# Kernel optimization log

Measured on AMD Instinct MI355X. Metric: run time of the kernel, lower is better.

## Reference

```python
import jax, jax.numpy as jnp
import numpy as np

B, TQ, TK, D, H = 4, 2048, 2048, 512, 8  # hidden=512, num_heads=8, head_dim=64


def setup_inputs() -> dict:
    key = jax.random.key(0)
    ks = jax.random.split(key, 7)
    s = 0.03  # small init scale for linear weights
    return {
        "q": jax.random.normal(ks[0], (B, TQ, D), jnp.float32),
        "k": jax.random.normal(ks[1], (B, TK, D), jnp.float32),
        "v": jax.random.normal(ks[2], (B, TK, D), jnp.float32),
        "Wq": jax.random.normal(ks[3], (D, D), jnp.float32) * s,
        "bq": jnp.zeros((D,), jnp.float32),
        "Wk": jax.random.normal(ks[4], (D, D), jnp.float32) * s,
        "bk": jnp.zeros((D,), jnp.float32),
        "Wv": jax.random.normal(ks[5], (D, D), jnp.float32) * s,
        "bv": jnp.zeros((D,), jnp.float32),
        "Wo": jax.random.normal(ks[6], (D, D), jnp.float32) * s,
        "bo": jnp.zeros((D,), jnp.float32),
    }


def reference(q, k, v, Wq, bq, Wk, bk, Wv, bv, Wo, bo):
    Bq, Tq, _ = q.shape
    Tk = k.shape[1]
    Dh = D // H  # head dim = 64
    # torch Linear: x @ W.T + b; split heads -> [B, H, T, Dh]
    qh = (q @ Wq.T + bq).reshape(Bq, Tq, H, Dh).transpose(0, 2, 1, 3)
    kh = (k @ Wk.T + bk).reshape(Bq, Tk, H, Dh).transpose(0, 2, 1, 3)
    vh = (v @ Wv.T + bv).reshape(Bq, Tk, H, Dh).transpose(0, 2, 1, 3)
    scale = 1.0 / float(np.sqrt(Dh))
    scores = jnp.einsum("bhqd,bhkd->bhqk", qh, kh) * scale  # [B,H,Tq,Tk]
    # causal mask: tril(ones, diagonal=Tk-Tq); log-additive masking == -inf off-band
    causal = jnp.tril(jnp.ones((Tq, Tk), bool), k=Tk - Tq)
    scores = jnp.where(causal, scores, -jnp.inf)
    w = jax.nn.softmax(scores, axis=-1)  # attention weights
    x = jnp.einsum("bhqk,bhkd->bhqd", w, vh)
    x = x.transpose(0, 2, 1, 3).reshape(Bq, Tq, D)
    return x @ Wo.T + bo, w
```

## Files before the change

### kernel.cpp

```cpp
#include <hip/hip_runtime.h>


typedef __attribute__((ext_vector_type(4))) float f32x4;
typedef __attribute__((ext_vector_type(8))) short short8;
typedef __attribute__((ext_vector_type(8))) __bf16 bf16x8;
typedef __attribute__((ext_vector_type(2))) unsigned int uintx2;
typedef __attribute__((ext_vector_type(4))) unsigned int uintx4;

static __device__ __forceinline__ unsigned short bfc(float f) {
  return __builtin_bit_cast(unsigned short, (__bf16)f);
}
static __device__ __forceinline__ unsigned pkbf(float a, float b) {
  return (unsigned)bfc(a) | ((unsigned)bfc(b) << 16);
}
static __device__ __forceinline__ short8 cvt_bf8(f32x4 f0, f32x4 f1) {
  uintx4 u;
  u[0] = pkbf(f0[0], f0[1]);
  u[1] = pkbf(f0[2], f0[3]);
  u[2] = pkbf(f1[0], f1[1]);
  u[3] = pkbf(f1[2], f1[3]);
  return __builtin_bit_cast(short8, u);
}

static __device__ __forceinline__ f32x4 mfma16(short8 a, short8 b, f32x4 c) {
  return __builtin_amdgcn_mfma_f32_16x16x32_bf16(
      __builtin_bit_cast(bf16x8, a), __builtin_bit_cast(bf16x8, b), c, 0, 0, 0);
}

#define GLD16(gsrc, ldst)                                                     \
  __builtin_amdgcn_global_load_lds(                                           \
      (const __attribute__((address_space(1))) void*)(gsrc),                  \
      (__attribute__((address_space(3))) void*)(ldst), 16, 0, 0)

template <int IN_BF16>
__device__ __forceinline__ void gemm_core(const void* __restrict__ Xv,
                                          const float* __restrict__ W,
                                          short (*As)[72], short (*Bs)[72],
                                          int row0, int col0, f32x4 (&acc)[4][4]) {
  const int tid = threadIdx.x;
  const int lane = tid & 63;
  const int wv = tid >> 6, wm = wv >> 1, wn = wv & 1;
  const int g = lane >> 4, c = lane & 15;

  for (int k0 = 0; k0 < 512; k0 += 64) {
    for (int ch = tid; ch < 1024; ch += 256) {
      const int r = ch >> 3, kc = (ch & 7) * 8;
      if (IN_BF16) {
        *(short8*)&As[r][kc] =
            *(const short8*)((const short*)Xv + (size_t)(row0 + r) * 512 + k0 + kc);
      } else {
        const float* src = (const float*)Xv + (size_t)(row0 + r) * 512 + k0 + kc;
        *(short8*)&As[r][kc] = cvt_bf8(*(const f32x4*)src, *(const f32x4*)(src + 4));
      }
      {
        const float* src = W + (size_t)(col0 + r) * 512 + k0 + kc;
        *(short8*)&Bs[r][kc] = cvt_bf8(*(const f32x4*)src, *(const f32x4*)(src + 4));
      }
    }
    __syncthreads();
#pragma unroll
    for (int kk = 0; kk < 2; ++kk) {
      short8 a[4], b[4];
#pragma unroll
      for (int i = 0; i < 4; ++i) a[i] = *(const short8*)&As[wm * 64 + i * 16 + c][kk * 32 + g * 8];
#pragma unroll
      for (int i = 0; i < 4; ++i) b[i] = *(const short8*)&Bs[wn * 64 + i * 16 + c][kk * 32 + g * 8];
#pragma unroll
      for (int mi = 0; mi < 4; ++mi)
#pragma unroll
        for (int ni = 0; ni < 4; ++ni) acc[mi][ni] = mfma16(a[mi], b[ni], acc[mi][ni]);
    }
    __syncthreads();
  }
}

__global__ __launch_bounds__(256) void qkv_gemm(
    const float* __restrict__ q, const float* __restrict__ k, const float* __restrict__ v,
    const float* __restrict__ Wq, const float* __restrict__ bq,
    const float* __restrict__ Wk, const float* __restrict__ bk,
    const float* __restrict__ Wv, const float* __restrict__ bv,
    unsigned short* __restrict__ Qbf, unsigned short* __restrict__ Kbf,
    unsigned short* __restrict__ Vbf) {
  __shared__ short As[128][72];
  __shared__ short Bs[128][72];
  const int z = blockIdx.z;
  const float* X = z == 0 ? q : (z == 1 ? k : v);
  const float* W = z == 0 ? Wq : (z == 1 ? Wk : Wv);
  const float* bias = z == 0 ? bq : (z == 1 ? bk : bv);
  const int row0 = blockIdx.x * 128, col0 = blockIdx.y * 128;

  f32x4 acc[4][4] = {};
  gemm_core<0>(X, W, As, Bs, row0, col0, acc);

  const int lane = threadIdx.x & 63;
  const int wv = threadIdx.x >> 6, wm = wv >> 1, wn = wv & 1;
  const int g = lane >> 4, c = lane & 15;

  if (z < 2) {
    unsigned short* Y = z == 0 ? Qbf : Kbf;
    const float scl = z == 0 ? 0.18033688f : 1.0f;
#pragma unroll
    for (int mi = 0; mi < 4; ++mi)
#pragma unroll
      for (int ni = 0; ni < 4; ++ni) {
        const int col = col0 + wn * 64 + ni * 16 + c;
        const float bvl = bias[col];
        const int rowb = row0 + wm * 64 + mi * 16 + g * 4;
#pragma unroll
        for (int r = 0; r < 4; ++r) {
          const int row = rowb + r;
          const int bb = row >> 11, t = row & 2047;
          const int h = col >> 6, dh = col & 63;
          Y[((size_t)((bb * 8 + h) * 2048 + t) << 6) + dh] = bfc((acc[mi][ni][r] + bvl) * scl);
        }
      }
  } else {
#pragma unroll
    for (int mi = 0; mi < 4; ++mi)
#pragma unroll
      for (int ni = 0; ni < 4; ++ni) {
        const int col = col0 + wn * 64 + ni * 16 + c;
        const float bvl = bias[col];
        const int rowb = row0 + wm * 64 + mi * 16 + g * 4;
        const int bb = rowb >> 11, t = rowb & 2047;
        const int h = col >> 6, dh = col & 63;
        uintx2 pk;
        pk[0] = pkbf(acc[mi][ni][0] + bvl, acc[mi][ni][1] + bvl);
        pk[1] = pkbf(acc[mi][ni][2] + bvl, acc[mi][ni][3] + bvl);
        *(uintx2*)(Vbf + ((size_t)((bb * 8 + h) * 64 + dh) * 2048 + t)) = pk;
      }
  }
}

__global__ __launch_bounds__(256) void out_gemm(const unsigned short* __restrict__ ctx,
                                                const float* __restrict__ Wo,
                                                const float* __restrict__ bo,
                                                float* __restrict__ out) {
  __shared__ short As[128][72];
  __shared__ short Bs[128][72];
  const int row0 = blockIdx.x * 128, col0 = blockIdx.y * 128;
  f32x4 acc[4][4] = {};
  gemm_core<1>(ctx, Wo, As, Bs, row0, col0, acc);

  const int lane = threadIdx.x & 63;
  const int wv = threadIdx.x >> 6, wm = wv >> 1, wn = wv & 1;
  const int g = lane >> 4, c = lane & 15;
#pragma unroll
  for (int mi = 0; mi < 4; ++mi)
#pragma unroll
    for (int ni = 0; ni < 4; ++ni) {
      const int col = col0 + wn * 64 + ni * 16 + c;
      const float bvl = bo[col];
      const int rowb = row0 + wm * 64 + mi * 16 + g * 4;
#pragma unroll
      for (int r = 0; r < 4; ++r) out[(size_t)(rowb + r) * 512 + col] = acc[mi][ni][r] + bvl;
    }
}

__global__ __launch_bounds__(256) void attn_kernel(
    const unsigned short* __restrict__ Qb, const unsigned short* __restrict__ Kb,
    const unsigned short* __restrict__ Vtg, unsigned short* __restrict__ ctx,
    float* __restrict__ wout) {
  __shared__ short Kd[2][8192];
  __shared__ short Vd[2][8192];
  __shared__ short Ps[4][16][128];

  const int tid = threadIdx.x, lane = tid & 63, wv = tid >> 6;
  const int g = lane >> 4, c = lane & 15;
  const int sw = (c & 7) << 3;
  const int p = blockIdx.x, bh = blockIdx.y;
  const unsigned short* Qp = Qb + (size_t)bh * (2048 * 64);
  const unsigned short* Kp = Kb + (size_t)bh * (2048 * 64);
  const unsigned short* Vp = Vtg + (size_t)bh * (64 * 2048);
  const int b_ = bh >> 3, h_ = bh & 7;

  for (int half = 0; half < 2; ++half) {
    const int t = half ? (31 - p) : p;
    const int q0 = t * 64;
    const int jmax = t >> 1;
    const int qr = q0 + wv * 16 + c;

    __syncthreads();
#pragma unroll
    for (int i = 0; i < 4; ++i) {
      const int gr = (wv * 4 + i) * 64 + lane;
      const int row = gr >> 3, slot = gr & 7;
      GLD16(Kp + ((size_t)row * 64) + ((slot ^ (row & 7)) << 3),
            (char*)Kd[0] + ((wv * 4 + i) << 10));
    }
#pragma unroll
    for (int i = 0; i < 4; ++i) {
      const int gr = (wv * 4 + i) * 64 + lane;
      const int row = gr >> 4, slot = gr & 15;
      GLD16(Vp + ((size_t)row * 2048) + ((slot ^ (row & 7)) << 3),
            (char*)Vd[0] + ((wv * 4 + i) << 10));
    }

    short8 qf[2];
    qf[0] = *(const short8*)(Qp + (size_t)qr * 64 + g * 8);
    qf[1] = *(const short8*)(Qp + (size_t)qr * 64 + 32 + g * 8);

    f32x4 O[4] = {};
    float l_r = 0.0f;

    for (int j = 0; j <= jmax; ++j) {
      __syncthreads();
      if (j < jmax) {
        const int nb = (j + 1) & 1;
#pragma unroll
        for (int i = 0; i < 4; ++i) {
          const int gr = (wv * 4 + i) * 64 + lane;
          const int row = gr >> 3, slot = gr & 7;
          GLD16(Kp + ((size_t)((j + 1) * 128 + row) * 64) + ((slot ^ (row & 7)) << 3),
                (char*)Kd[nb] + ((wv * 4 + i) << 10));
        }
#pragma unroll
        for (int i = 0; i < 4; ++i) {
          const int gr = (wv * 4 + i) * 64 + lane;
          const int row = gr >> 4, slot = gr & 15;
          GLD16(Vp + ((size_t)row * 2048) + (j + 1) * 128 + ((slot ^ (row & 7)) << 3),
                (char*)Vd[nb] + ((wv * 4 + i) << 10));
        }
      }
      const short* Ksb = Kd[j & 1];
      const short* Vsb = Vd[j & 1];

      f32x4 S[8];
#pragma unroll
      for (int nc = 0; nc < 8; ++nc) S[nc] = (f32x4){0.f, 0.f, 0.f, 0.f};
#pragma unroll
      for (int kk = 0; kk < 2; ++kk)
#pragma unroll
        for (int nc = 0; nc < 8; ++nc) {
          const int row = nc * 16 + c;
          const short8 kf = *(const short8*)&Ksb[row * 64 + (((kk * 4 + g) ^ (c & 7)) << 3)];
          S[nc] = mfma16(kf, qf[kk], S[nc]);
        }

      f32x4 ssum = {0.f, 0.f, 0.f, 0.f};
      if (j == jmax) {
        const int kvb = j * 128 + g * 4;
#pragma unroll
        for (int nc = 0; nc < 8; ++nc) {
#pragma unroll
          for (int r = 0; r < 4; ++r) {
            float val = __builtin_amdgcn_exp2f(S[nc][r]);
            if (kvb + nc * 16 + r > qr) val = 0.f;
            S[nc][r] = val;
          }
          ssum += S[nc];
        }
      } else {
#pragma unroll
        for (int nc = 0; nc < 8; ++nc) {
#pragma unroll
          for (int r = 0; r < 4; ++r) S[nc][r] = __builtin_amdgcn_exp2f(S[nc][r]);
          ssum += S[nc];
        }
      }
      l_r += ssum[0] + ssum[1] + ssum[2] + ssum[3];

#pragma unroll
      for (int nc = 0; nc < 8; ++nc) {
        uintx2 pk;
        pk[0] = pkbf(S[nc][0], S[nc][1]);
        pk[1] = pkbf(S[nc][2], S[nc][3]);
        *(uintx2*)&Ps[wv][c][(nc * 16 + g * 4) ^ sw] = pk;
      }

#pragma unroll
      for (int kk2 = 0; kk2 < 4; ++kk2) {
        const short8 pa = *(const short8*)&Ps[wv][c][(kk2 * 32 + g * 8) ^ sw];
#pragma unroll
        for (int nd = 0; nd < 4; ++nd) {
          const int row = nd * 16 + c;
          const short8 vb = *(const short8*)&Vsb[row * 128 + (((kk2 * 4 + g) ^ (c & 7)) << 3)];
          O[nd] = mfma16(pa, vb, O[nd]);
        }
      }
    }

    l_r += __shfl_xor(l_r, 16);
    l_r += __shfl_xor(l_r, 32);

    {
      float lv[4];
#pragma unroll
      for (int r = 0; r < 4; ++r) lv[r] = __shfl(l_r, g * 4 + r);
#pragma unroll
      for (int r = 0; r < 4; ++r) {
        const float inv = 1.0f / lv[r];
        const int trow = q0 + wv * 16 + g * 4 + r;
        unsigned short* cp = ctx + ((size_t)(b_ * 2048 + trow) * 512) + h_ * 64;
#pragma unroll
        for (int nd = 0; nd < 4; ++nd) cp[nd * 16 + c] = bfc(O[nd][r] * inv);
      }
    }

    const float inv_l = 1.0f / l_r;
    float* wbase = wout + ((size_t)bh * 2048 + q0) * 2048;
    for (int j = jmax; j >= 0; --j) {
      __syncthreads();
      if (j > 0) {
#pragma unroll
        for (int i = 0; i < 4; ++i) {
          const int gr = (wv * 4 + i) * 64 + lane;
          const int row = gr >> 3, slot = gr & 7;
          GLD16(Kp + ((size_t)((j - 1) * 128 + row) * 64) + ((slot ^ (row & 7)) << 3),
                (char*)Kd[(j - 1) & 1] + ((wv * 4 + i) << 10));
        }
      }
      const short* Ksb = Kd[j & 1];

      f32x4 S[8];
#pragma unroll
      for (int nc = 0; nc < 8; ++nc) S[nc] = (f32x4){0.f, 0.f, 0.f, 0.f};
#pragma unroll
      for (int kk = 0; kk < 2; ++kk)
#pragma unroll
        for (int nc = 0; nc < 8; ++nc) {
          const int row = nc * 16 + c;
          const short8 kf = *(const short8*)&Ksb[row * 64 + (((kk * 4 + g) ^ (c & 7)) << 3)];
          S[nc] = mfma16(kf, qf[kk], S[nc]);
        }

      const bool lastj = (j == jmax);
      float* wr = wbase + (size_t)(wv * 16 + c) * 2048 + j * 128;
#pragma unroll
      for (int nc = 0; nc < 8; ++nc) {
        f32x4 w4;
#pragma unroll
        for (int r = 0; r < 4; ++r) {
          float val = __builtin_amdgcn_exp2f(S[nc][r]) * inv_l;
          if (lastj && (j * 128 + nc * 16 + g * 4 + r > qr)) val = 0.f;
          w4[r] = val;
        }
        *(f32x4*)(wr + nc * 16 + g * 4) = w4;
      }
    }

    {
      const int c0 = (jmax + 1) * 128;
      const f32x4 z = {0.f, 0.f, 0.f, 0.f};
      for (int rr = wv; rr < 64; rr += 4) {
        float* rp = wbase + (size_t)rr * 2048;
        for (int x = c0 + lane * 4; x < 2048; x += 256) *(f32x4*)(rp + x) = z;
      }
    }
  }
}

extern "C" void kernel_launch(void* const* d_in, const int* in_sizes, int n_in,
                              void* d_out, int out_size, void* d_ws, size_t ws_size,
                              hipStream_t stream) {
  const float* q  = (const float*)d_in[0];
  const float* k  = (const float*)d_in[1];
  const float* v  = (const float*)d_in[2];
  const float* Wq = (const float*)d_in[3];
  const float* bq = (const float*)d_in[4];
  const float* Wk = (const float*)d_in[5];
  const float* bk = (const float*)d_in[6];
  const float* Wv = (const float*)d_in[7];
  const float* bv = (const float*)d_in[8];
  const float* Wo = (const float*)d_in[9];
  const float* bo = (const float*)d_in[10];

  unsigned short* Qbf = (unsigned short*)d_ws;
  unsigned short* Kbf = Qbf + (size_t)4194304;
  unsigned short* Vbf = Kbf + (size_t)4194304;
  unsigned short* ctx = Vbf + (size_t)4194304;

  float* out  = (float*)d_out;
  float* wout = out + (size_t)4 * 2048 * 512;

  qkv_gemm<<<dim3(64, 4, 3), 256, 0, stream>>>(q, k, v, Wq, bq, Wk, bk, Wv, bv, Qbf, Kbf, Vbf);
  attn_kernel<<<dim3(16, 32), 256, 0, stream>>>(Qbf, Kbf, Vbf, ctx, wout);
  out_gemm<<<dim3(64, 4), 256, 0, stream>>>(ctx, Wo, bo, out);
}
```

Before: 240.1 us.

## Pre-convert inputs to bf16, use async LDS loads in GEMMs, restructure attention grid

A separate conversion kernel turns the q/k/v activations and the projection weights into bf16, staging them in the attention-weights output buffer before it is overwritten. The QKV and output GEMMs then load their bf16 tiles straight into swizzled LDS with global_load_lds. The attention kernel drops the paired-tile scheme for one query tile per block on a larger grid with launch_bounds occupancy 3. It also reads V and the second-pass K directly from global memory instead of through LDS. The aim is less conversion work inside the GEMMs and higher attention occupancy, at the cost of an extra pass over the inputs and uncached global V/K loads.

```diff
diff --git a/kernel.cpp b/kernel.cpp
--- a/kernel.cpp
+++ b/kernel.cpp
@@ -32,39 +32,50 @@
       (const __attribute__((address_space(1))) void*)(gsrc),                  \
       (__attribute__((address_space(3))) void*)(ldst), 16, 0, 0)
 
-template <int IN_BF16>
-__device__ __forceinline__ void gemm_core(const void* __restrict__ Xv,
-                                          const float* __restrict__ W,
-                                          short (*As)[72], short (*Bs)[72],
-                                          int row0, int col0, f32x4 (&acc)[4][4]) {
-  const int tid = threadIdx.x;
-  const int lane = tid & 63;
+__global__ __launch_bounds__(256) void cvt_kernel(
+    const float* __restrict__ q, const float* __restrict__ k, const float* __restrict__ v,
+    const float* __restrict__ Wq, const float* __restrict__ Wk, const float* __restrict__ Wv,
+    unsigned short* __restrict__ dst) {
+  const int seg = blockIdx.y;
+  const float* src = seg == 0 ? q : seg == 1 ? k : seg == 2 ? v
+                     : seg == 3 ? Wq : seg == 4 ? Wk : Wv;
+  const size_t base = seg < 3 ? (size_t)seg * 4194304
+                              : 12582912ull + (size_t)(seg - 3) * 262144;
+  const size_t n = seg < 3 ? 4194304 : 262144;
+  const size_t i = ((size_t)blockIdx.x * 256 + threadIdx.x) * 8;
+  if (i < n) {
+    const f32x4 f0 = *(const f32x4*)(src + i), f1 = *(const f32x4*)(src + i + 4);
+    *(short8*)(dst + base + i) = cvt_bf8(f0, f1);
+  }
+}
+
+__device__ __forceinline__ void gemm_bf(const unsigned short* __restrict__ Xb,
+                                        const unsigned short* __restrict__ Wb,
+                                        short* As, short* Bs,
+                                        int row0, int col0, f32x4 (&acc)[4][4]) {
+  const int tid = threadIdx.x, lane = tid & 63;
   const int wv = tid >> 6, wm = wv >> 1, wn = wv & 1;
-  const int g = lane >> 4, c = lane & 15;
+  const int g = lane >> 4, c = lane & 15, sw = c & 7;
 
   for (int k0 = 0; k0 < 512; k0 += 64) {
-    for (int ch = tid; ch < 1024; ch += 256) {
-      const int r = ch >> 3, kc = (ch & 7) * 8;
-      if (IN_BF16) {
-        *(short8*)&As[r][kc] =
-            *(const short8*)((const short*)Xv + (size_t)(row0 + r) * 512 + k0 + kc);
-      } else {
-        const float* src = (const float*)Xv + (size_t)(row0 + r) * 512 + k0 + kc;
-        *(short8*)&As[r][kc] = cvt_bf8(*(const f32x4*)src, *(const f32x4*)(src + 4));
-      }
-      {
-        const float* src = W + (size_t)(col0 + r) * 512 + k0 + kc;
-        *(short8*)&Bs[r][kc] = cvt_bf8(*(const f32x4*)src, *(const f32x4*)(src + 4));
-      }
+#pragma unroll
+    for (int i = 0; i < 4; ++i) {
+      const int gr = (wv * 4 + i) * 64 + lane;
+      const int r = gr >> 3, s = gr & 7;
+      GLD16(Xb + (size_t)(row0 + r) * 512 + k0 + ((s ^ (r & 7)) << 3),
+            (char*)As + ((wv * 4 + i) << 10));
+      GLD16(Wb + (size_t)(col0 + r) * 512 + k0 + ((s ^ (r & 7)) << 3),
+            (char*)Bs + ((wv * 4 + i) << 10));
     }
     __syncthreads();
 #pragma unroll
     for (int kk = 0; kk < 2; ++kk) {
       short8 a[4], b[4];
 #pragma unroll
-      for (int i = 0; i < 4; ++i) a[i] = *(const short8*)&As[wm * 64 + i * 16 + c][kk * 32 + g * 8];
-#pragma unroll
-      for (int i = 0; i < 4; ++i) b[i] = *(const short8*)&Bs[wn * 64 + i * 16 + c][kk * 32 + g * 8];
+      for (int i = 0; i < 4; ++i) {
+        a[i] = *(const short8*)&As[((wm * 64 + i * 16 + c) << 6) + (((kk * 4 + g) ^ sw) << 3)];
+        b[i] = *(const short8*)&Bs[((wn * 64 + i * 16 + c) << 6) + (((kk * 4 + g) ^ sw) << 3)];
+      }
 #pragma unroll
       for (int mi = 0; mi < 4; ++mi)
 #pragma unroll
@@ -75,22 +86,20 @@
 }
 
 __global__ __launch_bounds__(256) void qkv_gemm(
-    const float* __restrict__ q, const float* __restrict__ k, const float* __restrict__ v,
-    const float* __restrict__ Wq, const float* __restrict__ bq,
-    const float* __restrict__ Wk, const float* __restrict__ bk,
-    const float* __restrict__ Wv, const float* __restrict__ bv,
+    const unsigned short* __restrict__ stash,
+    const float* __restrict__ bq, const float* __restrict__ bk, const float* __restrict__ bv,
     unsigned short* __restrict__ Qbf, unsigned short* __restrict__ Kbf,
     unsigned short* __restrict__ Vbf) {
-  __shared__ short As[128][72];
-  __shared__ short Bs[128][72];
+  __shared__ short As[128 * 64];
+  __shared__ short Bs[128 * 64];
   const int z = blockIdx.z;
-  const float* X = z == 0 ? q : (z == 1 ? k : v);
-  const float* W = z == 0 ? Wq : (z == 1 ? Wk : Wv);
+  const unsigned short* Xb = stash + (size_t)z * 4194304;
+  const unsigned short* Wb = stash + 12582912ull + (size_t)z * 262144;
   const float* bias = z == 0 ? bq : (z == 1 ? bk : bv);
   const int row0 = blockIdx.x * 128, col0 = blockIdx.y * 128;
 
   f32x4 acc[4][4] = {};
-  gemm_core<0>(X, W, As, Bs, row0, col0, acc);
+  gemm_bf(Xb, Wb, As, Bs, row0, col0, acc);
 
   const int lane = threadIdx.x & 63;
   const int wv = threadIdx.x >> 6, wm = wv >> 1, wn = wv & 1;
@@ -136,15 +145,44 @@
                                                 const float* __restrict__ Wo,
                                                 const float* __restrict__ bo,
                                                 float* __restrict__ out) {
-  __shared__ short As[128][72];
+  __shared__ short As[128 * 64];
   __shared__ short Bs[128][72];
+  const int tid = threadIdx.x, lane = tid & 63;
+  const int wv = tid >> 6, wm = wv >> 1, wn = wv & 1;
+  const int g = lane >> 4, c = lane & 15, sw = c & 7;
   const int row0 = blockIdx.x * 128, col0 = blockIdx.y * 128;
+
   f32x4 acc[4][4] = {};
-  gemm_core<1>(ctx, Wo, As, Bs, row0, col0, acc);
-
-  const int lane = threadIdx.x & 63;
-  const int wv = threadIdx.x >> 6, wm = wv >> 1, wn = wv & 1;
-  const int g = lane >> 4, c = lane & 15;
+  for (int k0 = 0; k0 < 512; k0 += 64) {
+#pragma unroll
+    for (int i = 0; i < 4; ++i) {
+      const int gr = (wv * 4 + i) * 64 + lane;
+      const int r = gr >> 3, s = gr & 7;
+      GLD16(ctx + (size_t)(row0 + r) * 512 + k0 + ((s ^ (r & 7)) << 3),
+            (char*)As + ((wv * 4 + i) << 10));
+    }
+    for (int ch = tid; ch < 1024; ch += 256) {
+      const int r = ch >> 3, kc = (ch & 7) * 8;
+      const float* src = Wo + (size_t)(col0 + r) * 512 + k0 + kc;
+      *(short8*)&Bs[r][kc] = cvt_bf8(*(const f32x4*)src, *(const f32x4*)(src + 4));
+    }
+    __syncthreads();
+#pragma unroll
+    for (int kk = 0; kk < 2; ++kk) {
+      short8 a[4], b[4];
+#pragma unroll
+      for (int i = 0; i < 4; ++i) {
+        a[i] = *(const short8*)&As[((wm * 64 + i * 16 + c) << 6) + (((kk * 4 + g) ^ sw) << 3)];
+        b[i] = *(const short8*)&Bs[wn * 64 + i * 16 + c][kk * 32 + g * 8];
+      }
+#pragma unroll
+      for (int mi = 0; mi < 4; ++mi)
+#pragma unroll
+        for (int ni = 0; ni < 4; ++ni) acc[mi][ni] = mfma16(a[mi], b[ni], acc[mi][ni]);
+    }
+    __syncthreads();
+  }
+
 #pragma unroll
   for (int mi = 0; mi < 4; ++mi)
 #pragma unroll
@@ -157,195 +195,163 @@
     }
 }
 
-__global__ __launch_bounds__(256) void attn_kernel(
+__global__ __launch_bounds__(256, 3) void attn_kernel(
     const unsigned short* __restrict__ Qb, const unsigned short* __restrict__ Kb,
     const unsigned short* __restrict__ Vtg, unsigned short* __restrict__ ctx,
     float* __restrict__ wout) {
   __shared__ short Kd[2][8192];
-  __shared__ short Vd[2][8192];
   __shared__ short Ps[4][16][128];
 
   const int tid = threadIdx.x, lane = tid & 63, wv = tid >> 6;
   const int g = lane >> 4, c = lane & 15;
   const int sw = (c & 7) << 3;
-  const int p = blockIdx.x, bh = blockIdx.y;
+  const int t = 31 - blockIdx.x, bh = blockIdx.y;
   const unsigned short* Qp = Qb + (size_t)bh * (2048 * 64);
   const unsigned short* Kp = Kb + (size_t)bh * (2048 * 64);
   const unsigned short* Vp = Vtg + (size_t)bh * (64 * 2048);
   const int b_ = bh >> 3, h_ = bh & 7;
 
-  for (int half = 0; half < 2; ++half) {
-    const int t = half ? (31 - p) : p;
-    const int q0 = t * 64;
-    const int jmax = t >> 1;
-    const int qr = q0 + wv * 16 + c;
-
-    __syncthreads();
-#pragma unroll
-    for (int i = 0; i < 4; ++i) {
-      const int gr = (wv * 4 + i) * 64 + lane;
-      const int row = gr >> 3, slot = gr & 7;
-      GLD16(Kp + ((size_t)row * 64) + ((slot ^ (row & 7)) << 3),
-            (char*)Kd[0] + ((wv * 4 + i) << 10));
-    }
-#pragma unroll
-    for (int i = 0; i < 4; ++i) {
-      const int gr = (wv * 4 + i) * 64 + lane;
-      const int row = gr >> 4, slot = gr & 15;
-      GLD16(Vp + ((size_t)row * 2048) + ((slot ^ (row & 7)) << 3),
-            (char*)Vd[0] + ((wv * 4 + i) << 10));
-    }
-
-    short8 qf[2];
-    qf[0] = *(const short8*)(Qp + (size_t)qr * 64 + g * 8);
-    qf[1] = *(const short8*)(Qp + (size_t)qr * 64 + 32 + g * 8);
-
-    f32x4 O[4] = {};
-    float l_r = 0.0f;
-
-    for (int j = 0; j <= jmax; ++j) {
-      __syncthreads();
-      if (j < jmax) {
-        const int nb = (j + 1) & 1;
-#pragma unroll
-        for (int i = 0; i < 4; ++i) {
-          const int gr = (wv * 4 + i) * 64 + lane;
-          const int row = gr >> 3, slot = gr & 7;
-          GLD16(Kp + ((size_t)((j + 1) * 128 + row) * 64) + ((slot ^ (row & 7)) << 3),
-                (char*)Kd[nb] + ((wv * 4 + i) << 10));
+  const int q0 = t * 64;
+  const int jmax = t >> 1;
+  const int qr = q0 + wv * 16 + c;
+
+#pragma unroll
+  for (int i = 0; i < 4; ++i) {
+    const int gr = (wv * 4 + i) * 64 + lane;
+    const int row = gr >> 3, slot = gr & 7;
+    GLD16(Kp + ((size_t)row * 64) + ((slot ^ (row & 7)) << 3),
+          (char*)Kd[0] + ((wv * 4 + i) << 10));
+  }
+
+  short8 qf[2];
+  qf[0] = *(const short8*)(Qp + (size_t)qr * 64 + g * 8);
+  qf[1] = *(const short8*)(Qp + (size_t)qr * 64 + 32 + g * 8);
+
+  f32x4 O[4] = {};
+  float l_r = 0.0f;
+
+  for (int j = 0; j <= jmax; ++j) {
+    __syncthreads();
+    if (j < jmax) {
+      const int nb = (j + 1) & 1;
+#pragma unroll
+      for (int i = 0; i < 4; ++i) {
+        const int gr = (wv * 4 + i) * 64 + lane;
+        const int row = gr >> 3, slot = gr & 7;
+        GLD16(Kp + ((size_t)((j + 1) * 128 + row) * 64) + ((slot ^ (row & 7)) << 3),
+              (char*)Kd[nb] + ((wv * 4 + i) << 10));
+      }
+    }
+    const short* Ksb = Kd[j & 1];
+
+    f32x4 S[8];
+#pragma unroll
+    for (int nc = 0; nc < 8; ++nc) S[nc] = (f32x4){0.f, 0.f, 0.f, 0.f};
+#pragma unroll
+    for (int kk = 0; kk < 2; ++kk)
+#pragma unroll
+      for (int nc = 0; nc < 8; ++nc) {
+        const int row = nc * 16 + c;
+        const short8 kf = *(const short8*)&Ksb[row * 64 + (((kk * 4 + g) ^ (c & 7)) << 3)];
+        S[nc] = mfma16(kf, qf[kk], S[nc]);
+      }
+
+    f32x4 ssum = {0.f, 0.f, 0.f, 0.f};
+    if (j == jmax) {
+      const int kvb = j * 128 + g * 4;
+#pragma unroll
+      for (int nc = 0; nc < 8; ++nc) {
+#pragma unroll
+        for (int r = 0; r < 4; ++r) {
+          float val = __builtin_amdgcn_exp2f(S[nc][r]);
+          if (kvb + nc * 16 + r > qr) val = 0.f;
+          S[nc][r] = val;
         }
-#pragma unroll
-        for (int i = 0; i < 4; ++i) {
-          const int gr = (wv * 4 + i) * 64 + lane;
-          const int row = gr >> 4, slot = gr & 15;
-          GLD16(Vp + ((size_t)row * 2048) + (j + 1) * 128 + ((slot ^ (row & 7)) << 3),
-                (char*)Vd[nb] + ((wv * 4 + i) << 10));
-        }
-      }
-      const short* Ksb = Kd[j & 1];
-      const short* Vsb = Vd[j & 1];
-
-      f32x4 S[8];
-#pragma unroll
-      for (int nc = 0; nc < 8; ++nc) S[nc] = (f32x4){0.f, 0.f, 0.f, 0.f};
-#pragma unroll
-      for (int kk = 0; kk < 2; ++kk)
-#pragma unroll
-        for (int nc = 0; nc < 8; ++nc) {
-          const int row = nc * 16 + c;
-          const short8 kf = *(const short8*)&Ksb[row * 64 + (((kk * 4 + g) ^ (c & 7)) << 3)];
-          S[nc] = mfma16(kf, qf[kk], S[nc]);
-        }
-
-      f32x4 ssum = {0.f, 0.f, 0.f, 0.f};
-      if (j == jmax) {
-        const int kvb = j * 128 + g * 4;
-#pragma unroll
-        for (int nc = 0; nc < 8; ++nc) {
-#pragma unroll
-          for (int r = 0; r < 4; ++r) {
-            float val = __builtin_amdgcn_exp2f(S[nc][r]);
-            if (kvb + nc * 16 + r > qr) val = 0.f;
-            S[nc][r] = val;
-          }
-          ssum += S[nc];
-        }
-      } else {
-#pragma unroll
-        for (int nc = 0; nc < 8; ++nc) {
-#pragma unroll
-          for (int r = 0; r < 4; ++r) S[nc][r] = __builtin_amdgcn_exp2f(S[nc][r]);
-          ssum += S[nc];
-        }
-      }
-      l_r += ssum[0] + ssum[1] + ssum[2] + ssum[3];
-
+        ssum += S[nc];
+      }
+    } else {
 #pragma unroll
       for (int nc = 0; nc < 8; ++nc) {
-        uintx2 pk;
-        pk[0] = pkbf(S[nc][0], S[nc][1]);
-        pk[1] = pkbf(S[nc][2], S[nc][3]);
-        *(uintx2*)&Ps[wv][c][(nc * 16 + g * 4) ^ sw] = pk;
-      }
-
-#pragma unroll
-      for (int kk2 = 0; kk2 < 4; ++kk2) {
-        const short8 pa = *(const short8*)&Ps[wv][c][(kk2 * 32 + g * 8) ^ sw];
-#pragma unroll
-        for (int nd = 0; nd < 4; ++nd) {
-          const int row = nd * 16 + c;
-          const short8 vb = *(const short8*)&Vsb[row * 128 + (((kk2 * 4 + g) ^ (c & 7)) << 3)];
-          O[nd] = mfma16(pa, vb, O[nd]);
-        }
-      }
-    }
-
-    l_r += __shfl_xor(l_r, 16);
-    l_r += __shfl_xor(l_r, 32);
-
-    {
-      float lv[4];
-#pragma unroll
-      for (int r = 0; r < 4; ++r) lv[r] = __shfl(l_r, g * 4 + r);
+#pragma unroll
+        for (int r = 0; r < 4; ++r) S[nc][r] = __builtin_amdgcn_exp2f(S[nc][r]);
+        ssum += S[nc];
+      }
+    }
+    l_r += ssum[0] + ssum[1] + ssum[2] + ssum[3];
+
+#pragma unroll
+    for (int nc = 0; nc < 8; ++nc) {
+      uintx2 pk;
+      pk[0] = pkbf(S[nc][0], S[nc][1]);
+      pk[1] = pkbf(S[nc][2], S[nc][3]);
+      *(uintx2*)&Ps[wv][c][(nc * 16 + g * 4) ^ sw] = pk;
+    }
+
+#pragma unroll
+    for (int kk2 = 0; kk2 < 4; ++kk2) {
+      const short8 pa = *(const short8*)&Ps[wv][c][(kk2 * 32 + g * 8) ^ sw];
+#pragma unroll
+      for (int nd = 0; nd < 4; ++nd) {
+        const short8 vb = *(const short8*)(Vp + (size_t)(nd * 16 + c) * 2048 +
+                                           j * 128 + kk2 * 32 + g * 8);
+        O[nd] = mfma16(pa, vb, O[nd]);
+      }
+    }
+  }
+
+  l_r += __shfl_xor(l_r, 16);
+  l_r += __shfl_xor(l_r, 32);
+
+  {
+    float lv[4];
+#pragma unroll
+    for (int r = 0; r < 4; ++r) lv[r] = __shfl(l_r, g * 4 + r);
+#pragma unroll
+    for (int r = 0; r < 4; ++r) {
+      const float inv = 1.0f / lv[r];
+      const int trow = q0 + wv * 16 + g * 4 + r;
+      unsigned short* cp = ctx + ((size_t)(b_ * 2048 + trow) * 512) + h_ * 64;
+#pragma unroll
+      for (int nd = 0; nd < 4; ++nd) cp[nd * 16 + c] = bfc(O[nd][r] * inv);
+    }
+  }
+
+  const float inv_l = 1.0f / l_r;
+  float* wbase = wout + ((size_t)bh * 2048 + q0) * 2048;
+  for (int j = 0; j <= jmax; ++j) {
+    f32x4 S[8];
+#pragma unroll
+    for (int nc = 0; nc < 8; ++nc) S[nc] = (f32x4){0.f, 0.f, 0.f, 0.f};
+#pragma unroll
+    for (int kk = 0; kk < 2; ++kk)
+#pragma unroll
+      for (int nc = 0; nc < 8; ++nc) {
+        const short8 kf = *(const short8*)(Kp + (size_t)(j * 128 + nc * 16 + c) * 64 +
+                                           kk * 32 + g * 8);
+        S[nc] = mfma16(kf, qf[kk], S[nc]);
+      }
+
+    const bool lastj = (j == jmax);
+    float* wr = wbase + (size_t)(wv * 16 + c) * 2048 + j * 128;
+#pragma unroll
+    for (int nc = 0; nc < 8; ++nc) {
+      f32x4 w4;
 #pragma unroll
       for (int r = 0; r < 4; ++r) {
-        const float inv = 1.0f / lv[r];
-        const int trow = q0 + wv * 16 + g * 4 + r;
-        unsigned short* cp = ctx + ((size_t)(b_ * 2048 + trow) * 512) + h_ * 64;
-#pragma unroll
-        for (int nd = 0; nd < 4; ++nd) cp[nd * 16 + c] = bfc(O[nd][r] * inv);
-      }
-    }
-
-    const float inv_l = 1.0f / l_r;
-    float* wbase = wout + ((size_t)bh * 2048 + q0) * 2048;
-    for (int j = jmax; j >= 0; --j) {
-      __syncthreads();
-      if (j > 0) {
-#pragma unroll
-        for (int i = 0; i < 4; ++i) {
-          const int gr = (wv * 4 + i) * 64 + lane;
-          const int row = gr >> 3, slot = gr & 7;
-          GLD16(Kp + ((size_t)((j - 1) * 128 + row) * 64) + ((slot ^ (row & 7)) << 3),
-                (char*)Kd[(j - 1) & 1] + ((wv * 4 + i) << 10));
-        }
-      }
-      const short* Ksb = Kd[j & 1];
-
-      f32x4 S[8];
-#pragma unroll
-      for (int nc = 0; nc < 8; ++nc) S[nc] = (f32x4){0.f, 0.f, 0.f, 0.f};
-#pragma unroll
-      for (int kk = 0; kk < 2; ++kk)
-#pragma unroll
-        for (int nc = 0; nc < 8; ++nc) {
-          const int row = nc * 16 + c;
-          const short8 kf = *(const short8*)&Ksb[row * 64 + (((kk * 4 + g) ^ (c & 7)) << 3)];
-          S[nc] = mfma16(kf, qf[kk], S[nc]);
-        }
-
-      const bool lastj = (j == jmax);
-      float* wr = wbase + (size_t)(wv * 16 + c) * 2048 + j * 128;
-#pragma unroll
-      for (int nc = 0; nc < 8; ++nc) {
-        f32x4 w4;
-#pragma unroll
-        for (int r = 0; r < 4; ++r) {
-          float val = __builtin_amdgcn_exp2f(S[nc][r]) * inv_l;
-          if (lastj && (j * 128 + nc * 16 + g * 4 + r > qr)) val = 0.f;
-          w4[r] = val;
-        }
-        *(f32x4*)(wr + nc * 16 + g * 4) = w4;
-      }
-    }
-
-    {
-      const int c0 = (jmax + 1) * 128;
-      const f32x4 z = {0.f, 0.f, 0.f, 0.f};
-      for (int rr = wv; rr < 64; rr += 4) {
-        float* rp = wbase + (size_t)rr * 2048;
-        for (int x = c0 + lane * 4; x < 2048; x += 256) *(f32x4*)(rp + x) = z;
-      }
+        float val = __builtin_amdgcn_exp2f(S[nc][r]) * inv_l;
+        if (lastj && (j * 128 + nc * 16 + g * 4 + r > qr)) val = 0.f;
+        w4[r] = val;
+      }
+      *(f32x4*)(wr + nc * 16 + g * 4) = w4;
+    }
+  }
+
+  {
+    const int c0 = (jmax + 1) * 128;
+    const f32x4 z = {0.f, 0.f, 0.f, 0.f};
+    for (int rr = wv; rr < 64; rr += 4) {
+      float* rp = wbase + (size_t)rr * 2048;
+      for (int x = c0 + lane * 4; x < 2048; x += 256) *(f32x4*)(rp + x) = z;
     }
   }
 }
@@ -372,8 +378,10 @@
 
   float* out  = (float*)d_out;
   float* wout = out + (size_t)4 * 2048 * 512;
-
-  qkv_gemm<<<dim3(64, 4, 3), 256, 0, stream>>>(q, k, v, Wq, bq, Wk, bk, Wv, bv, Qbf, Kbf, Vbf);
-  attn_kernel<<<dim3(16, 32), 256, 0, stream>>>(Qbf, Kbf, Vbf, ctx, wout);
+  unsigned short* stash = (unsigned short*)wout;
+
+  cvt_kernel<<<dim3(2048, 6), 256, 0, stream>>>(q, k, v, Wq, Wk, Wv, stash);
+  qkv_gemm<<<dim3(64, 4, 3), 256, 0, stream>>>(stash, bq, bk, bv, Qbf, Kbf, Vbf);
+  attn_kernel<<<dim3(32, 32), 256, 0, stream>>>(Qbf, Kbf, Vbf, ctx, wout);
   out_gemm<<<dim3(64, 4), 256, 0, stream>>>(ctx, Wo, bo, out);
 }
```

After: 413.8 us. 1.72x slower.
